# Kernel tuning notes

Hardware: AMD Instinct MI355X
Metric: run time of the kernel (lower is better)

Reference implementation:

```python
import jax, jax.numpy as jnp
import numpy as np


def gcn_conv(x, edge_index, W, b):
    # PyG GCNConv: h = x @ W; add self-loops; symmetric D^-1/2 (A+I) D^-1/2 aggregation; + bias
    n = x.shape[0]
    h = x @ W  # [N, out]
    loop = jnp.arange(n, dtype=edge_index.dtype)
    src = jnp.concatenate([edge_index[0], loop])  # message sources
    dst = jnp.concatenate([edge_index[1], loop])  # message targets
    ones = jnp.ones(dst.shape[0], dtype=h.dtype)
    deg = jax.ops.segment_sum(ones, dst, num_segments=n)  # in-degree incl. self-loop
    dinv = jnp.where(deg > 0, jax.lax.rsqrt(deg), 0.0)
    norm = dinv[src] * dinv[dst]  # [E+N]
    msg = h[src] * norm[:, None]  # gather + scale
    out = jax.ops.segment_sum(msg, dst, num_segments=n)  # scatter-add
    return out + b


def setup_inputs() -> dict:
    key = jax.random.key(0)
    ks = jax.random.split(key, 6)
    N, E, D = 100000, 600000, 128
    x = jax.random.normal(ks[0], (N, D), dtype=jnp.float32)
    edge_index = jax.random.randint(ks[1], (2, E), 0, N, dtype=jnp.int64)
    s = 1.0 / np.sqrt(D)
    W1 = jax.random.normal(ks[2], (D, D), dtype=jnp.float32) * s
    b1 = jnp.zeros((D,), dtype=jnp.float32)
    W2 = jax.random.normal(ks[3], (2 * D, D), dtype=jnp.float32) * (1.0 / np.sqrt(2 * D))
    b2 = jnp.zeros((D,), dtype=jnp.float32)
    Wout = jax.random.normal(ks[4], (D, 1), dtype=jnp.float32) * s
    bout = jnp.zeros((1,), dtype=jnp.float32)
    return {"x": x, "edge_index": edge_index, "W1": W1, "b1": b1,
            "W2": W2, "b2": b2, "Wout": Wout, "bout": bout}


def reference(x, edge_index, W1, b1, W2, b2, Wout, bout):
    y = gcn_conv(x, edge_index, W1, b1)          # [N, D]
    y = jnp.concatenate([x, y], axis=-1)          # [N, 2D]
    y = jax.nn.leaky_relu(y, negative_slope=0.01)
    z = gcn_conv(y, edge_index, W2, b2)           # [N, D]
    z = jax.nn.leaky_relu(z, negative_slope=0.01)
    return z @ Wout + bout                        # [N, 1]
```

## Files before the change

### kernel.cpp

```cpp
#include <hip/hip_runtime.h>

#define DIM 128
#define CAP 48

typedef _Float16 half8 __attribute__((ext_vector_type(8)));
typedef float f32x4 __attribute__((ext_vector_type(4)));

__device__ __forceinline__ float lrelu(float v) { return v > 0.f ? v : 0.01f * v; }

__device__ __forceinline__ void gather_sum(
    const _Float16* __restrict__ H, const int* __restrict__ sl,
    int cnt, int g, int zr, float a[8]) {
    int c16 = cnt < 16 ? cnt : 16;
    int sidb = (g < c16) ? sl[g] : zr;
    half8 v[8];
#pragma unroll
    for (int j = 0; j < 8; ++j) {
        int s = __shfl(sidb, j, 16);
        v[j] = *(const half8*)&H[(size_t)s * DIM + g * 8];
    }
#pragma unroll
    for (int j = 0; j < 8; ++j)
#pragma unroll
        for (int e = 0; e < 8; ++e) a[e] += (float)v[j][e];
    if (cnt > 8) {
#pragma unroll
        for (int j = 0; j < 8; ++j) {
            int s = __shfl(sidb, 8 + j, 16);
            v[j] = *(const half8*)&H[(size_t)s * DIM + g * 8];
        }
#pragma unroll
        for (int j = 0; j < 8; ++j)
#pragma unroll
            for (int e = 0; e < 8; ++e) a[e] += (float)v[j][e];
        if (cnt > 16) {
            for (int base = 16; base < cnt; base += 16) {
                int m = cnt - base;
                if (m > 16) m = 16;
                int sb = (g < m) ? sl[base + g] : zr;
                for (int j = 0; j < m; ++j) {
                    int s = __shfl(sb, j, 16);
                    half8 vv = *(const half8*)&H[(size_t)s * DIM + g * 8];
#pragma unroll
                    for (int e = 0; e < 8; ++e) a[e] += (float)vv[e];
                }
            }
        }
    }
}

__device__ __forceinline__ void gather_sum_scaled(
    const _Float16* __restrict__ H, const int* __restrict__ cursor,
    const int* __restrict__ sl, int cnt, int g, int zr, float a[8]) {
    int c16 = cnt < 16 ? cnt : 16;
    int sidb = (g < c16) ? sl[g] : zr;
    float dvb = rsqrtf((float)cursor[sidb] + 1.0f);
    half8 v[8];
#pragma unroll
    for (int j = 0; j < 8; ++j) {
        int s = __shfl(sidb, j, 16);
        v[j] = *(const half8*)&H[(size_t)s * DIM + g * 8];
    }
#pragma unroll
    for (int j = 0; j < 8; ++j) {
        float sc = __shfl(dvb, j, 16);
#pragma unroll
        for (int e = 0; e < 8; ++e) a[e] = fmaf((float)v[j][e], sc, a[e]);
    }
    if (cnt > 8) {
#pragma unroll
        for (int j = 0; j < 8; ++j) {
            int s = __shfl(sidb, 8 + j, 16);
            v[j] = *(const half8*)&H[(size_t)s * DIM + g * 8];
        }
#pragma unroll
        for (int j = 0; j < 8; ++j) {
            float sc = __shfl(dvb, 8 + j, 16);
#pragma unroll
            for (int e = 0; e < 8; ++e) a[e] = fmaf((float)v[j][e], sc, a[e]);
        }
        if (cnt > 16) {
            for (int base = 16; base < cnt; base += 16) {
                int m = cnt - base;
                if (m > 16) m = 16;
                int sb = (g < m) ? sl[base + g] : zr;
                float db2 = rsqrtf((float)cursor[sb] + 1.0f);
                for (int j = 0; j < m; ++j) {
                    int s = __shfl(sb, j, 16);
                    float sc = __shfl(db2, j, 16);
                    half8 vv = *(const half8*)&H[(size_t)s * DIM + g * 8];
#pragma unroll
                    for (int e = 0; e < 8; ++e) a[e] = fmaf((float)vv[e], sc, a[e]);
                }
            }
        }
    }
}

__global__ __launch_bounds__(256) void k_init(
    int* __restrict__ cursor, int na, int nzb,
    const float* __restrict__ W1, _Float16* __restrict__ Wp1,
    const float* __restrict__ W2, _Float16* __restrict__ Wp2,
    _Float16* __restrict__ zrow) {
    int b = blockIdx.x;
    if (b < nzb) {
        int i = b * 256 + threadIdx.x;
        if (i < na) cursor[i] = 0;
        return;
    }
    b -= nzb;
    if (b >= 192) {
        if (threadIdx.x < 16) {
            half8 z = 0;
            *(half8*)&zrow[threadIdx.x * 8] = z;
        }
        return;
    }
    const float* W;
    _Float16* Wp;
    int tid2;
    if (b < 64) { W = W1; Wp = Wp1; tid2 = b * 256 + threadIdx.x; }
    else        { W = W2; Wp = Wp2; tid2 = (b - 64) * 256 + threadIdx.x; }
    int jj = tid2 & 7;
    int frag = tid2 >> 3;
    int l = frag & 63;
    int cb = (frag >> 6) & 7;
    int kb = frag >> 9;
    Wp[tid2] = (_Float16)W[(size_t)(kb * 32 + ((l >> 4) << 3) + jj) * DIM + cb * 16 + (l & 15)];
}

__global__ __launch_bounds__(256, 2) void k_front(
    const float* __restrict__ x, const _Float16* __restrict__ Wp1,
    const _Float16* __restrict__ Wp2, _Float16* __restrict__ hs,
    _Float16* __restrict__ P, int n, int gb,
    const int* __restrict__ esrc, const int* __restrict__ edst,
    int* __restrict__ cursor, int* __restrict__ srcs, int E) {
    __shared__ _Float16 Hs[64 * 136];
    const int bb = blockIdx.x;
    if (bb >= gb) {
        int i = (bb - gb) * 256 + threadIdx.x;
        if (i < E) {
            int d = edst[i];
            int p = atomicAdd(&cursor[d], 1);
            if (p < CAP) srcs[(size_t)d * CAP + p] = esrc[i];
        }
        return;
    }
    const int tid = threadIdx.x;
    const int w = tid >> 6, l = tid & 63;
    const int row0 = bb * 64;
    const int arow = row0 + w * 16 + (l & 15);
    const int kq = (l >> 4) << 3;
    const bool ok = arow < n;
    const float* xr = &x[(size_t)arow * DIM + kq];

    f32x4 ah[8], ap[8];
#pragma unroll
    for (int cb = 0; cb < 8; ++cb) {
        f32x4 z = {0.f, 0.f, 0.f, 0.f};
        ah[cb] = z; ap[cb] = z;
    }

#pragma unroll
    for (int kb = 0; kb < 4; ++kb) {
        float4 v0 = make_float4(0.f, 0.f, 0.f, 0.f), v1 = v0;
        if (ok) {
            v0 = *(const float4*)&xr[kb * 32];
            v1 = *(const float4*)&xr[kb * 32 + 4];
        }
        half8 a, al;
        a[0] = (_Float16)v0.x; a[1] = (_Float16)v0.y;
        a[2] = (_Float16)v0.z; a[3] = (_Float16)v0.w;
        a[4] = (_Float16)v1.x; a[5] = (_Float16)v1.y;
        a[6] = (_Float16)v1.z; a[7] = (_Float16)v1.w;
#pragma unroll
        for (int e = 0; e < 8; ++e) {
            _Float16 t = a[e];
            al[e] = (t > (_Float16)0.f) ? t : t * (_Float16)0.01f;
        }
#pragma unroll
        for (int cb = 0; cb < 8; ++cb) {
            half8 bf = *(const half8*)&Wp1[((kb * 8 + cb) * 64 + l) * 8];
            ah[cb] = __builtin_amdgcn_mfma_f32_16x16x32_f16(a, bf, ah[cb], 0, 0, 0);
        }
#pragma unroll
        for (int cb = 0; cb < 8; ++cb) {
            half8 bf = *(const half8*)&Wp2[((kb * 8 + cb) * 64 + l) * 8];
            ap[cb] = __builtin_amdgcn_mfma_f32_16x16x32_f16(al, bf, ap[cb], 0, 0, 0);
        }
    }
    const int orow = w * 16 + ((l >> 4) << 2);
    const int oc = l & 15;
#pragma unroll
    for (int reg = 0; reg < 4; ++reg) {
#pragma unroll
        for (int cb = 0; cb < 8; ++cb)
            Hs[(orow + reg) * 136 + cb * 16 + oc] = (_Float16)ah[cb][reg];
    }
    __syncthreads();
#pragma unroll
    for (int it = 0; it < 4; ++it) {
        int i = it * 256 + tid;
        int r = i >> 4, c = (i & 15) * 8;
        if (row0 + r < n)
            *(half8*)&hs[(size_t)(row0 + r) * DIM + c] = *(const half8*)&Hs[r * 136 + c];
    }
    _Float16* pl = P + ((size_t)(bb * 4 + w) * 64 + l) * 32;
#pragma unroll
    for (int c = 0; c < 4; ++c) {
        half8 o;
#pragma unroll
        for (int e = 0; e < 4; ++e) {
            o[e]     = (_Float16)ap[2 * c][e];
            o[4 + e] = (_Float16)ap[2 * c + 1][e];
        }
        *(half8*)&pl[c * 8] = o;
    }
}

__global__ __launch_bounds__(256, 2) void k_mm2g(
    const _Float16* __restrict__ hs, const int* __restrict__ cursor,
    const int* __restrict__ srcs, const float* __restrict__ b1,
    const _Float16* __restrict__ Wp2, const _Float16* __restrict__ P,
    _Float16* __restrict__ hs2, int n) {
    __shared__ _Float16 LS[64 * 136];
    const int tid = threadIdx.x;
    const int w = tid >> 6, l = tid & 63;
    const int g = tid & 15, gid = tid >> 4;
    const int row0 = blockIdx.x * 64;

    f32x4 acc[8];
    const _Float16* pl = P + ((size_t)(blockIdx.x * 4 + w) * 64 + l) * 32;
#pragma unroll
    for (int c = 0; c < 4; ++c) {
        half8 pv = *(const half8*)&pl[c * 8];
#pragma unroll
        for (int e = 0; e < 4; ++e) {
            acc[2 * c][e]     = (float)pv[e];
            acc[2 * c + 1][e] = (float)pv[4 + e];
        }
    }

#pragma unroll
    for (int it = 0; it < 4; ++it) {
        int node = row0 + it * 16 + gid;
        half8 o = 0;
        if (node < n) {
            int rawc = cursor[node];
            int cnt = rawc > CAP ? CAP : rawc;
            const int* sl = &srcs[(size_t)node * CAP];
            float d = rsqrtf((float)rawc + 1.0f);
            half8 h = *(const half8*)&hs[(size_t)node * DIM + g * 8];
            float a[8];
#pragma unroll
            for (int e = 0; e < 8; ++e) a[e] = (float)h[e] * d;
            gather_sum_scaled(hs, cursor, sl, cnt, g, n, a);
            const float4 bb0 = *(const float4*)&b1[g * 8];
            const float4 bb1 = *(const float4*)&b1[g * 8 + 4];
            o[0] = (_Float16)lrelu(fmaf(a[0], d, bb0.x));
            o[1] = (_Float16)lrelu(fmaf(a[1], d, bb0.y));
            o[2] = (_Float16)lrelu(fmaf(a[2], d, bb0.z));
            o[3] = (_Float16)lrelu(fmaf(a[3], d, bb0.w));
            o[4] = (_Float16)lrelu(fmaf(a[4], d, bb1.x));
            o[5] = (_Float16)lrelu(fmaf(a[5], d, bb1.y));
            o[6] = (_Float16)lrelu(fmaf(a[6], d, bb1.z));
            o[7] = (_Float16)lrelu(fmaf(a[7], d, bb1.w));
        }
        *(half8*)&LS[(((it * 4 + (g >> 2)) * 64) + (g & 3) * 16 + gid) * 8] = o;
    }
    __syncthreads();

#pragma unroll
    for (int kb = 0; kb < 4; ++kb) {
        half8 a = *(const half8*)&LS[((w * 4 + kb) * 64 + l) * 8];
#pragma unroll
        for (int cb = 0; cb < 8; ++cb) {
            half8 bf = *(const half8*)&Wp2[(((kb + 4) * 8 + cb) * 64 + l) * 8];
            acc[cb] = __builtin_amdgcn_mfma_f32_16x16x32_f16(a, bf, acc[cb], 0, 0, 0);
        }
    }
    __syncthreads();
    const int orow = w * 16 + ((l >> 4) << 2);
    const int oc = l & 15;
#pragma unroll
    for (int reg = 0; reg < 4; ++reg) {
        int grow = row0 + orow + reg;
        float d = (grow < n) ? rsqrtf((float)cursor[grow] + 1.0f) : 0.f;
#pragma unroll
        for (int cb = 0; cb < 8; ++cb)
            LS[(orow + reg) * 136 + cb * 16 + oc] = (_Float16)(acc[cb][reg] * d);
    }
    __syncthreads();
#pragma unroll
    for (int it = 0; it < 4; ++it) {
        int i = it * 256 + tid;
        int r = i >> 4, c = (i & 15) * 8;
        if (row0 + r < n)
            *(half8*)&hs2[(size_t)(row0 + r) * DIM + c] = *(const half8*)&LS[r * 136 + c];
    }
}

__global__ __launch_bounds__(256) void k_gather2(
    const _Float16* __restrict__ hs2, const int* __restrict__ cursor,
    const int* __restrict__ srcs, const float* __restrict__ b2,
    const float* __restrict__ wout, const float* __restrict__ bout,
    float* __restrict__ out, int n) {
    const int node = blockIdx.x * 16 + (threadIdx.x >> 4);
    const int g = threadIdx.x & 15;
    if (node >= n) return;
    int rawc = cursor[node];
    int cnt = rawc > CAP ? CAP : rawc;
    const int* sl = &srcs[(size_t)node * CAP];
    half8 h = *(const half8*)&hs2[(size_t)node * DIM + g * 8];
    float a[8];
#pragma unroll
    for (int e = 0; e < 8; ++e) a[e] = (float)h[e];
    gather_sum(hs2, sl, cnt, g, n, a);
    float d = rsqrtf((float)rawc + 1.0f);
    const float4 bb0 = *(const float4*)&b2[g * 8];
    const float4 bb1 = *(const float4*)&b2[g * 8 + 4];
    const float4 wv0 = *(const float4*)&wout[g * 8];
    const float4 wv1 = *(const float4*)&wout[g * 8 + 4];
    float s = lrelu(fmaf(a[0], d, bb0.x)) * wv0.x + lrelu(fmaf(a[1], d, bb0.y)) * wv0.y +
              lrelu(fmaf(a[2], d, bb0.z)) * wv0.z + lrelu(fmaf(a[3], d, bb0.w)) * wv0.w +
              lrelu(fmaf(a[4], d, bb1.x)) * wv1.x + lrelu(fmaf(a[5], d, bb1.y)) * wv1.y +
              lrelu(fmaf(a[6], d, bb1.z)) * wv1.z + lrelu(fmaf(a[7], d, bb1.w)) * wv1.w;
#pragma unroll
    for (int off = 8; off > 0; off >>= 1) s += __shfl_down(s, off, 16);
    if (g == 0) out[node] = s + bout[0];
}

extern "C" void kernel_launch(void* const* d_in, const int* in_sizes, int n_in,
                              void* d_out, int out_size, void* d_ws, size_t ws_size,
                              hipStream_t stream) {
    const float* x    = (const float*)d_in[0];
    const int*   ei   = (const int*)d_in[1];
    const float* W1   = (const float*)d_in[2];
    const float* b1   = (const float*)d_in[3];
    const float* W2   = (const float*)d_in[4];
    const float* b2   = (const float*)d_in[5];
    const float* Wout = (const float*)d_in[6];
    const float* bout = (const float*)d_in[7];
    float* out = (float*)d_out;

    const int N = in_sizes[0] / DIM;
    const int E = in_sizes[1] / 2;
    const int* src = ei;
    const int* dst = ei + E;

    const int gb = (N + 63) / 64;
    const long long nx = (long long)N * DIM;

    size_t Na = ((size_t)N + 63) & ~(size_t)63;
    int* cursor   = (int*)d_ws;
    int* srcs     = cursor + Na;
    _Float16* Wp1 = (_Float16*)(srcs + (size_t)N * CAP);
    _Float16* Wp2 = Wp1 + 128 * 128;
    _Float16* hsb = Wp2 + 256 * 128;
    _Float16* Pb  = hsb + nx + DIM;

    const int eb = (E + 255) / 256;
    const int nzb = ((int)Na + 255) / 256;

    k_init<<<nzb + 193, 256, 0, stream>>>(cursor, (int)Na, nzb, W1, Wp1, W2, Wp2, hsb + nx);
    k_front<<<gb + eb, 256, 0, stream>>>(x, Wp1, Wp2, hsb, Pb, N, gb, src, dst, cursor, srcs, E);
    k_mm2g<<<gb, 256, 0, stream>>>(hsb, cursor, srcs, b1, Wp2, Pb, Pb, N);
    k_gather2<<<(N + 15) / 16, 256, 0, stream>>>(Pb, cursor, srcs, b2, Wout, bout, out, N);
}
```

Baseline: 217.7 us.

## Move x-half of second GEMM from front kernel into gather-GEMM kernel

Moves the leaky-relu(x) @ W2[:128] product out of k_front and recomputes it inside k_mm2g straight from x. This drops the intermediate P buffer write and read, and lightens k_front so it overlaps better with the edge-bucketing blocks. In exchange, k_mm2g now reads x in fp32 on top of the gathers and needs a separate hs2 output buffer with its own zero row. Cursor zeroing also switches to int4 vector stores.

```diff
diff --git a/kernel.cpp b/kernel.cpp
--- a/kernel.cpp
+++ b/kernel.cpp
@@ -98,14 +98,17 @@
 }
 
 __global__ __launch_bounds__(256) void k_init(
-    int* __restrict__ cursor, int na, int nzb,
+    int* __restrict__ cursor, int na4, int nzb,
     const float* __restrict__ W1, _Float16* __restrict__ Wp1,
     const float* __restrict__ W2, _Float16* __restrict__ Wp2,
-    _Float16* __restrict__ zrow) {
+    _Float16* __restrict__ zrow, _Float16* __restrict__ zrow2) {
     int b = blockIdx.x;
     if (b < nzb) {
         int i = b * 256 + threadIdx.x;
-        if (i < na) cursor[i] = 0;
+        if (i < na4) {
+            int4 z = make_int4(0, 0, 0, 0);
+            *(int4*)&cursor[i * 4] = z;
+        }
         return;
     }
     b -= nzb;
@@ -113,6 +116,7 @@
         if (threadIdx.x < 16) {
             half8 z = 0;
             *(half8*)&zrow[threadIdx.x * 8] = z;
+            *(half8*)&zrow2[threadIdx.x * 8] = z;
         }
         return;
     }
@@ -131,8 +135,7 @@
 
 __global__ __launch_bounds__(256, 2) void k_front(
     const float* __restrict__ x, const _Float16* __restrict__ Wp1,
-    const _Float16* __restrict__ Wp2, _Float16* __restrict__ hs,
-    _Float16* __restrict__ P, int n, int gb,
+    _Float16* __restrict__ hs, int n, int gb,
     const int* __restrict__ esrc, const int* __restrict__ edst,
     int* __restrict__ cursor, int* __restrict__ srcs, int E) {
     __shared__ _Float16 Hs[64 * 136];
@@ -154,11 +157,11 @@
     const bool ok = arow < n;
     const float* xr = &x[(size_t)arow * DIM + kq];
 
-    f32x4 ah[8], ap[8];
+    f32x4 ah[8];
 #pragma unroll
     for (int cb = 0; cb < 8; ++cb) {
         f32x4 z = {0.f, 0.f, 0.f, 0.f};
-        ah[cb] = z; ap[cb] = z;
+        ah[cb] = z;
     }
 
 #pragma unroll
@@ -168,25 +171,15 @@
             v0 = *(const float4*)&xr[kb * 32];
             v1 = *(const float4*)&xr[kb * 32 + 4];
         }
-        half8 a, al;
+        half8 a;
         a[0] = (_Float16)v0.x; a[1] = (_Float16)v0.y;
         a[2] = (_Float16)v0.z; a[3] = (_Float16)v0.w;
         a[4] = (_Float16)v1.x; a[5] = (_Float16)v1.y;
         a[6] = (_Float16)v1.z; a[7] = (_Float16)v1.w;
 #pragma unroll
-        for (int e = 0; e < 8; ++e) {
-            _Float16 t = a[e];
-            al[e] = (t > (_Float16)0.f) ? t : t * (_Float16)0.01f;
-        }
-#pragma unroll
         for (int cb = 0; cb < 8; ++cb) {
             half8 bf = *(const half8*)&Wp1[((kb * 8 + cb) * 64 + l) * 8];
             ah[cb] = __builtin_amdgcn_mfma_f32_16x16x32_f16(a, bf, ah[cb], 0, 0, 0);
-        }
-#pragma unroll
-        for (int cb = 0; cb < 8; ++cb) {
-            half8 bf = *(const half8*)&Wp2[((kb * 8 + cb) * 64 + l) * 8];
-            ap[cb] = __builtin_amdgcn_mfma_f32_16x16x32_f16(al, bf, ap[cb], 0, 0, 0);
         }
     }
     const int orow = w * 16 + ((l >> 4) << 2);
@@ -205,23 +198,12 @@
         if (row0 + r < n)
             *(half8*)&hs[(size_t)(row0 + r) * DIM + c] = *(const half8*)&Hs[r * 136 + c];
     }
-    _Float16* pl = P + ((size_t)(bb * 4 + w) * 64 + l) * 32;
-#pragma unroll
-    for (int c = 0; c < 4; ++c) {
-        half8 o;
-#pragma unroll
-        for (int e = 0; e < 4; ++e) {
-            o[e]     = (_Float16)ap[2 * c][e];
-            o[4 + e] = (_Float16)ap[2 * c + 1][e];
-        }
-        *(half8*)&pl[c * 8] = o;
-    }
 }
 
 __global__ __launch_bounds__(256, 2) void k_mm2g(
-    const _Float16* __restrict__ hs, const int* __restrict__ cursor,
-    const int* __restrict__ srcs, const float* __restrict__ b1,
-    const _Float16* __restrict__ Wp2, const _Float16* __restrict__ P,
+    const float* __restrict__ x, const _Float16* __restrict__ hs,
+    const int* __restrict__ cursor, const int* __restrict__ srcs,
+    const float* __restrict__ b1, const _Float16* __restrict__ Wp2,
     _Float16* __restrict__ hs2, int n) {
     __shared__ _Float16 LS[64 * 136];
     const int tid = threadIdx.x;
@@ -230,15 +212,10 @@
     const int row0 = blockIdx.x * 64;
 
     f32x4 acc[8];
-    const _Float16* pl = P + ((size_t)(blockIdx.x * 4 + w) * 64 + l) * 32;
-#pragma unroll
-    for (int c = 0; c < 4; ++c) {
-        half8 pv = *(const half8*)&pl[c * 8];
-#pragma unroll
-        for (int e = 0; e < 4; ++e) {
-            acc[2 * c][e]     = (float)pv[e];
-            acc[2 * c + 1][e] = (float)pv[4 + e];
-        }
+#pragma unroll
+    for (int cb = 0; cb < 8; ++cb) {
+        f32x4 z = {0.f, 0.f, 0.f, 0.f};
+        acc[cb] = z;
     }
 
 #pragma unroll
@@ -267,6 +244,36 @@
             o[7] = (_Float16)lrelu(fmaf(a[7], d, bb1.w));
         }
         *(half8*)&LS[(((it * 4 + (g >> 2)) * 64) + (g & 3) * 16 + gid) * 8] = o;
+    }
+
+    {
+        const int arow = row0 + w * 16 + (l & 15);
+        const int kq = (l >> 4) << 3;
+        const bool ok = arow < n;
+        const float* xr = &x[(size_t)arow * DIM + kq];
+#pragma unroll
+        for (int kb = 0; kb < 4; ++kb) {
+            float4 v0 = make_float4(0.f, 0.f, 0.f, 0.f), v1 = v0;
+            if (ok) {
+                v0 = *(const float4*)&xr[kb * 32];
+                v1 = *(const float4*)&xr[kb * 32 + 4];
+            }
+            half8 a, al;
+            a[0] = (_Float16)v0.x; a[1] = (_Float16)v0.y;
+            a[2] = (_Float16)v0.z; a[3] = (_Float16)v0.w;
+            a[4] = (_Float16)v1.x; a[5] = (_Float16)v1.y;
+            a[6] = (_Float16)v1.z; a[7] = (_Float16)v1.w;
+#pragma unroll
+            for (int e = 0; e < 8; ++e) {
+                _Float16 t = a[e];
+                al[e] = (t > (_Float16)0.f) ? t : t * (_Float16)0.01f;
+            }
+#pragma unroll
+            for (int cb = 0; cb < 8; ++cb) {
+                half8 bf = *(const half8*)&Wp2[((kb * 8 + cb) * 64 + l) * 8];
+                acc[cb] = __builtin_amdgcn_mfma_f32_16x16x32_f16(al, bf, acc[cb], 0, 0, 0);
+            }
+        }
     }
     __syncthreads();
 
@@ -357,13 +364,15 @@
     _Float16* Wp1 = (_Float16*)(srcs + (size_t)N * CAP);
     _Float16* Wp2 = Wp1 + 128 * 128;
     _Float16* hsb = Wp2 + 256 * 128;
-    _Float16* Pb  = hsb + nx + DIM;
+    _Float16* hs2 = hsb + nx + DIM;
 
     const int eb = (E + 255) / 256;
-    const int nzb = ((int)Na + 255) / 256;
-
-    k_init<<<nzb + 193, 256, 0, stream>>>(cursor, (int)Na, nzb, W1, Wp1, W2, Wp2, hsb + nx);
-    k_front<<<gb + eb, 256, 0, stream>>>(x, Wp1, Wp2, hsb, Pb, N, gb, src, dst, cursor, srcs, E);
-    k_mm2g<<<gb, 256, 0, stream>>>(hsb, cursor, srcs, b1, Wp2, Pb, Pb, N);
-    k_gather2<<<(N + 15) / 16, 256, 0, stream>>>(Pb, cursor, srcs, b2, Wout, bout, out, N);
-}
+    const int na4 = (int)(Na / 4);
+    const int nzb = (na4 + 255) / 256;
+
+    k_init<<<nzb + 193, 256, 0, stream>>>(cursor, na4, nzb, W1, Wp1, W2, Wp2,
+                                          hsb + nx, hs2 + nx);
+    k_front<<<gb + eb, 256, 0, stream>>>(x, Wp1, hsb, N, gb, src, dst, cursor, srcs, E);
+    k_mm2g<<<gb, 256, 0, stream>>>(x, hsb, cursor, srcs, b1, Wp2, hs2, N);
+    k_gather2<<<(N + 15) / 16, 256, 0, stream>>>(hs2, cursor, srcs, b2, Wout, bout, out, N);
+}
```

After: 213.2 us. 1.02x faster.
